# Kernel optimization log

Hardware: AMD Instinct MI355X
Metric: run time of the kernel (lower is better)

The kernel has to match this reference:

```python
import jax, jax.numpy as jnp
import numpy as np

B, S, F = 4096, 128, 256

def setup_inputs() -> dict:
    key = jax.random.key(0)
    k0, k1, k2 = jax.random.split(key, 3)
    token_embeds = jax.random.normal(k0, (B, S, F), dtype=jnp.float32)
    attention_mask = jax.random.randint(k1, (B, S), 0, 2).astype(jnp.bool_)
    kw1, kw2 = jax.random.split(k2)
    scale = 1.0 / np.sqrt(F)
    W1 = jax.random.uniform(kw1, (F, F), minval=-scale, maxval=scale, dtype=jnp.float32)
    W2 = jax.random.uniform(kw2, (F, F), minval=-scale, maxval=scale, dtype=jnp.float32)
    b1 = jnp.zeros((F,), jnp.float32)
    b2 = jnp.zeros((F,), jnp.float32)
    return {"token_embeds": token_embeds, "attention_mask": attention_mask,
            "W1": W1, "b1": b1, "W2": W2, "b2": b2}

def reference(token_embeds, attention_mask, W1, b1, W2, b2):
    # masked sum pooling over tokens: [B,S,F] * [B,S,1] -> sum over S -> [B,F]
    mask = attention_mask.astype(token_embeds.dtype)[:, :, None]
    x = jnp.einsum('bsf,bs->bf', token_embeds, mask[:, :, 0])
    # linear1 + tanh (dropout is identity in eval mode)
    x = jnp.tanh(x @ W1.T + b1)
    x = jnp.tanh(x @ W2.T + b2)
    return x
```

## Files before the change

kernel.cpp:

```cpp
#include <hip/hip_runtime.h>
#include <stdint.h>
#include <math.h>

constexpr int S_LEN = 128;
constexpr int F_DIM = 256;
constexpr int F4    = F_DIM / 4;
constexpr int ROWS  = 16;

__global__ __launch_bounds__(256) void pool_kernel(
    const float* __restrict__ te, const void* __restrict__ mask,
    float* __restrict__ xout)
{
  const int t    = threadIdx.x;
  const int wave = t >> 6;
  const int lane = t & 63;
  const long b   = (long)blockIdx.x * 4 + wave;

  const uint32_t* mw = (const uint32_t*)mask;
  uint32_t v = mw[lane];
  unsigned long long isF  = __ballot(v == 0x3F800000u);
  unsigned long long big  = __ballot(v > 1u);
  const int fmt = isF ? 2 : (big ? 1 : 0);

  const float4* te4  = (const float4*)te;
  const long    tb   = b * S_LEN * F4 + lane;
  const long    mb   = b * S_LEN;

  float4 acc = make_float4(0.f, 0.f, 0.f, 0.f);

  if (fmt == 0) {
    const int* mi = (const int*)mask;
    #pragma unroll 4
    for (int s = 0; s < S_LEN; ++s) {
      float  m  = (float)mi[mb + s];
      float4 tv = te4[tb + (long)s * F4];
      acc.x = fmaf(m, tv.x, acc.x); acc.y = fmaf(m, tv.y, acc.y);
      acc.z = fmaf(m, tv.z, acc.z); acc.w = fmaf(m, tv.w, acc.w);
    }
  } else if (fmt == 1) {
    const uint8_t* mu = (const uint8_t*)mask;
    #pragma unroll 4
    for (int s = 0; s < S_LEN; ++s) {
      float  m  = (float)mu[mb + s];
      float4 tv = te4[tb + (long)s * F4];
      acc.x = fmaf(m, tv.x, acc.x); acc.y = fmaf(m, tv.y, acc.y);
      acc.z = fmaf(m, tv.z, acc.z); acc.w = fmaf(m, tv.w, acc.w);
    }
  } else {
    const float* mf = (const float*)mask;
    #pragma unroll 4
    for (int s = 0; s < S_LEN; ++s) {
      float  m  = mf[mb + s];
      float4 tv = te4[tb + (long)s * F4];
      acc.x = fmaf(m, tv.x, acc.x); acc.y = fmaf(m, tv.y, acc.y);
      acc.z = fmaf(m, tv.z, acc.z); acc.w = fmaf(m, tv.w, acc.w);
    }
  }

  ((float4*)xout)[b * F4 + lane] = acc;
}

__global__ __launch_bounds__(256) void mlp_kernel(
    float* __restrict__ x,
    const float* __restrict__ W1, const float* __restrict__ b1,
    const float* __restrict__ W2, const float* __restrict__ b2)
{
  __shared__ float xs[ROWS][F_DIM];
  __shared__ float wt[64][F_DIM];

  const int t    = threadIdx.x;
  const int wave = t >> 6;
  const int lane = t & 63;
  const long rowBase = (long)blockIdx.x * ROWS;
  float4* xg = (float4*)(x + rowBase * F_DIM);

  #pragma unroll
  for (int k = 0; k < (ROWS * F4) / 256; ++k)
    ((float4*)&xs[0][0])[t + 256 * k] = xg[t + 256 * k];
  __syncthreads();

  const int r0 = wave * (ROWS / 4);
  const int c  = lane * 4;

  for (int layer = 0; layer < 2; ++layer) {
    const float* W    = layer ? W2 : W1;
    const float* bias = layer ? b2 : b1;

    float4 bv = ((const float4*)bias)[lane];
    float4 acc[ROWS / 4];
    #pragma unroll
    for (int r = 0; r < ROWS / 4; ++r) acc[r] = bv;

    for (int fc = 0; fc < F_DIM; fc += 64) {
      __syncthreads();
      const float4* wrow = (const float4*)(W + (long)t * F_DIM + fc);
      #pragma unroll
      for (int k = 0; k < 16; ++k) {
        float4 wv = wrow[k];
        wt[4*k + 0][t] = wv.x; wt[4*k + 1][t] = wv.y;
        wt[4*k + 2][t] = wv.z; wt[4*k + 3][t] = wv.w;
      }
      __syncthreads();

      #pragma unroll 8
      for (int f = 0; f < 64; ++f) {
        float4 wv = *(const float4*)&wt[f][c];
        #pragma unroll
        for (int r = 0; r < ROWS / 4; ++r) {
          float xv = xs[r0 + r][fc + f];
          acc[r].x = fmaf(xv, wv.x, acc[r].x);
          acc[r].y = fmaf(xv, wv.y, acc[r].y);
          acc[r].z = fmaf(xv, wv.z, acc[r].z);
          acc[r].w = fmaf(xv, wv.w, acc[r].w);
        }
      }
    }
    __syncthreads();
    #pragma unroll
    for (int r = 0; r < ROWS / 4; ++r) {
      float4 o;
      o.x = tanhf(acc[r].x); o.y = tanhf(acc[r].y);
      o.z = tanhf(acc[r].z); o.w = tanhf(acc[r].w);
      *(float4*)&xs[r0 + r][c] = o;
    }
    __syncthreads();
  }

  #pragma unroll
  for (int k = 0; k < (ROWS * F4) / 256; ++k)
    xg[t + 256 * k] = ((float4*)&xs[0][0])[t + 256 * k];
}

extern "C" void kernel_launch(void* const* d_in, const int* in_sizes, int n_in,
                              void* d_out, int out_size, void* d_ws, size_t ws_size,
                              hipStream_t stream) {
  const float* te   = (const float*)d_in[0];
  const void*  mask = d_in[1];
  const float* W1   = (const float*)d_in[2];
  const float* b1   = (const float*)d_in[3];
  const float* W2   = (const float*)d_in[4];
  const float* b2   = (const float*)d_in[5];
  float* out = (float*)d_out;

  const int Btot = in_sizes[0] / (S_LEN * F_DIM);

  pool_kernel<<<dim3(Btot / 4), dim3(256), 0, stream>>>(te, mask, out);
  mlp_kernel<<<dim3(Btot / ROWS), dim3(256), 0, stream>>>(out, W1, b1, W2, b2);
}
```

Before: 724.1 us.

## Gather only unmasked tokens in pooling and pre-transpose weights for MLP

```diff
diff --git a/kernel.cpp b/kernel.cpp
--- a/kernel.cpp
+++ b/kernel.cpp
@@ -7,128 +7,134 @@
 constexpr int F4    = F_DIM / 4;
 constexpr int ROWS  = 16;
 
+__device__ __forceinline__ int mbcnt64(unsigned long long m) {
+  return __builtin_amdgcn_mbcnt_hi((unsigned)(m >> 32),
+         __builtin_amdgcn_mbcnt_lo((unsigned)(m & 0xffffffffu), 0));
+}
+__device__ __forceinline__ void add4(float4& a, const float4 b) {
+  a.x += b.x; a.y += b.y; a.z += b.z; a.w += b.w;
+}
+__device__ __forceinline__ void fma4(float4& a, float s, const float4 w) {
+  a.x = fmaf(s, w.x, a.x); a.y = fmaf(s, w.y, a.y);
+  a.z = fmaf(s, w.z, a.z); a.w = fmaf(s, w.w, a.w);
+}
+
+__global__ __launch_bounds__(256) void wt_kernel(
+    const float* __restrict__ W1, const float* __restrict__ W2,
+    float* __restrict__ wsT)
+{
+  int id  = blockIdx.x * 256 + threadIdx.x;
+  int mat = id >> 16;
+  int o   = id & 65535;
+  int f   = o >> 8, j = o & 255;
+  const float* W = mat ? W2 : W1;
+  wsT[(mat << 16) + o] = W[j * 256 + f];
+}
+
 __global__ __launch_bounds__(256) void pool_kernel(
     const float* __restrict__ te, const void* __restrict__ mask,
     float* __restrict__ xout)
 {
-  const int t    = threadIdx.x;
-  const int wave = t >> 6;
-  const int lane = t & 63;
-  const long b   = (long)blockIdx.x * 4 + wave;
+  __shared__ int sl[4][132];
+
+  const int t = threadIdx.x, w = t >> 6, l = t & 63;
+  const long b = (long)blockIdx.x * 4 + w;
 
   const uint32_t* mw = (const uint32_t*)mask;
-  uint32_t v = mw[lane];
-  unsigned long long isF  = __ballot(v == 0x3F800000u);
-  unsigned long long big  = __ballot(v > 1u);
-  const int fmt = isF ? 2 : (big ? 1 : 0);
+  uint32_t v = mw[l];
+  const int fmt = __ballot(v == 0x3F800000u) ? 2 : (__ballot(v > 1u) ? 1 : 0);
 
-  const float4* te4  = (const float4*)te;
-  const long    tb   = b * S_LEN * F4 + lane;
-  const long    mb   = b * S_LEN;
+  bool a0, a1;
+  if (fmt == 0) {
+    const int* m = (const int*)mask + b * S_LEN;
+    a0 = m[l] != 0; a1 = m[64 + l] != 0;
+  } else if (fmt == 1) {
+    const uint8_t* m = (const uint8_t*)mask + b * S_LEN;
+    a0 = m[l] != 0; a1 = m[64 + l] != 0;
+  } else {
+    const float* m = (const float*)mask + b * S_LEN;
+    a0 = m[l] != 0.f; a1 = m[64 + l] != 0.f;
+  }
+  unsigned long long b0 = __ballot(a0), b1 = __ballot(a1);
+  const int c0 = __popcll(b0);
+  const int cnt = c0 + __popcll(b1);
+  if (a0) sl[w][mbcnt64(b0)]      = l;
+  if (a1) sl[w][c0 + mbcnt64(b1)] = 64 + l;
+  __syncthreads();
 
+  const float4* src = (const float4*)te + b * (S_LEN * F4) + l;
   float4 acc = make_float4(0.f, 0.f, 0.f, 0.f);
 
-  if (fmt == 0) {
-    const int* mi = (const int*)mask;
-    #pragma unroll 4
-    for (int s = 0; s < S_LEN; ++s) {
-      float  m  = (float)mi[mb + s];
-      float4 tv = te4[tb + (long)s * F4];
-      acc.x = fmaf(m, tv.x, acc.x); acc.y = fmaf(m, tv.y, acc.y);
-      acc.z = fmaf(m, tv.z, acc.z); acc.w = fmaf(m, tv.w, acc.w);
-    }
-  } else if (fmt == 1) {
-    const uint8_t* mu = (const uint8_t*)mask;
-    #pragma unroll 4
-    for (int s = 0; s < S_LEN; ++s) {
-      float  m  = (float)mu[mb + s];
-      float4 tv = te4[tb + (long)s * F4];
-      acc.x = fmaf(m, tv.x, acc.x); acc.y = fmaf(m, tv.y, acc.y);
-      acc.z = fmaf(m, tv.z, acc.z); acc.w = fmaf(m, tv.w, acc.w);
-    }
-  } else {
-    const float* mf = (const float*)mask;
-    #pragma unroll 4
-    for (int s = 0; s < S_LEN; ++s) {
-      float  m  = mf[mb + s];
-      float4 tv = te4[tb + (long)s * F4];
-      acc.x = fmaf(m, tv.x, acc.x); acc.y = fmaf(m, tv.y, acc.y);
-      acc.z = fmaf(m, tv.z, acc.z); acc.w = fmaf(m, tv.w, acc.w);
-    }
+  int i = 0;
+  for (; i + 8 <= cnt; i += 8) {
+    int s0 = sl[w][i+0], s1 = sl[w][i+1], s2 = sl[w][i+2], s3 = sl[w][i+3];
+    int s4 = sl[w][i+4], s5 = sl[w][i+5], s6 = sl[w][i+6], s7 = sl[w][i+7];
+    float4 t0 = src[s0*F4], t1 = src[s1*F4], t2 = src[s2*F4], t3 = src[s3*F4];
+    float4 t4 = src[s4*F4], t5 = src[s5*F4], t6 = src[s6*F4], t7 = src[s7*F4];
+    add4(t0, t1); add4(t2, t3); add4(t4, t5); add4(t6, t7);
+    add4(t0, t2); add4(t4, t6); add4(t0, t4); add4(acc, t0);
   }
+  for (; i < cnt; ++i) add4(acc, src[sl[w][i] * F4]);
 
-  ((float4*)xout)[b * F4 + lane] = acc;
+  ((float4*)xout)[b * F4 + l] = acc;
 }
 
 __global__ __launch_bounds__(256) void mlp_kernel(
-    float* __restrict__ x,
-    const float* __restrict__ W1, const float* __restrict__ b1,
-    const float* __restrict__ W2, const float* __restrict__ b2)
+    float* __restrict__ x, const float* __restrict__ wsT,
+    const float* __restrict__ b1, const float* __restrict__ b2)
 {
   __shared__ float xs[ROWS][F_DIM];
   __shared__ float wt[64][F_DIM];
 
-  const int t    = threadIdx.x;
-  const int wave = t >> 6;
-  const int lane = t & 63;
+  const int t = threadIdx.x, w = t >> 6, l = t & 63;
   const long rowBase = (long)blockIdx.x * ROWS;
   float4* xg = (float4*)(x + rowBase * F_DIM);
 
   #pragma unroll
   for (int k = 0; k < (ROWS * F4) / 256; ++k)
-    ((float4*)&xs[0][0])[t + 256 * k] = xg[t + 256 * k];
+    ((float4*)xs)[t + 256 * k] = xg[t + 256 * k];
   __syncthreads();
 
-  const int r0 = wave * (ROWS / 4);
-  const int c  = lane * 4;
+  const int r0 = w * 4;
+  const int c  = l * 4;
 
   for (int layer = 0; layer < 2; ++layer) {
-    const float* W    = layer ? W2 : W1;
+    const float* Wt   = wsT + layer * 65536;
     const float* bias = layer ? b2 : b1;
 
-    float4 bv = ((const float4*)bias)[lane];
-    float4 acc[ROWS / 4];
-    #pragma unroll
-    for (int r = 0; r < ROWS / 4; ++r) acc[r] = bv;
+    float4 bv = ((const float4*)bias)[l];
+    float4 acc0 = bv, acc1 = bv, acc2 = bv, acc3 = bv;
 
     for (int fc = 0; fc < F_DIM; fc += 64) {
       __syncthreads();
-      const float4* wrow = (const float4*)(W + (long)t * F_DIM + fc);
+      const float4* src = (const float4*)(Wt + fc * F_DIM);
       #pragma unroll
-      for (int k = 0; k < 16; ++k) {
-        float4 wv = wrow[k];
-        wt[4*k + 0][t] = wv.x; wt[4*k + 1][t] = wv.y;
-        wt[4*k + 2][t] = wv.z; wt[4*k + 3][t] = wv.w;
-      }
+      for (int k = 0; k < 16; ++k)
+        ((float4*)wt)[t + 256 * k] = src[t + 256 * k];
       __syncthreads();
 
       #pragma unroll 8
       for (int f = 0; f < 64; ++f) {
         float4 wv = *(const float4*)&wt[f][c];
-        #pragma unroll
-        for (int r = 0; r < ROWS / 4; ++r) {
-          float xv = xs[r0 + r][fc + f];
-          acc[r].x = fmaf(xv, wv.x, acc[r].x);
-          acc[r].y = fmaf(xv, wv.y, acc[r].y);
-          acc[r].z = fmaf(xv, wv.z, acc[r].z);
-          acc[r].w = fmaf(xv, wv.w, acc[r].w);
-        }
+        float x0 = xs[r0+0][fc+f], x1 = xs[r0+1][fc+f];
+        float x2 = xs[r0+2][fc+f], x3 = xs[r0+3][fc+f];
+        fma4(acc0, x0, wv); fma4(acc1, x1, wv);
+        fma4(acc2, x2, wv); fma4(acc3, x3, wv);
       }
     }
+    float4 o0, o1, o2, o3;
+    o0.x=tanhf(acc0.x); o0.y=tanhf(acc0.y); o0.z=tanhf(acc0.z); o0.w=tanhf(acc0.w);
+    o1.x=tanhf(acc1.x); o1.y=tanhf(acc1.y); o1.z=tanhf(acc1.z); o1.w=tanhf(acc1.w);
+    o2.x=tanhf(acc2.x); o2.y=tanhf(acc2.y); o2.z=tanhf(acc2.z); o2.w=tanhf(acc2.w);
+    o3.x=tanhf(acc3.x); o3.y=tanhf(acc3.y); o3.z=tanhf(acc3.z); o3.w=tanhf(acc3.w);
     __syncthreads();
-    #pragma unroll
-    for (int r = 0; r < ROWS / 4; ++r) {
-      float4 o;
-      o.x = tanhf(acc[r].x); o.y = tanhf(acc[r].y);
-      o.z = tanhf(acc[r].z); o.w = tanhf(acc[r].w);
-      *(float4*)&xs[r0 + r][c] = o;
-    }
-    __syncthreads();
+    *(float4*)&xs[r0+0][c] = o0; *(float4*)&xs[r0+1][c] = o1;
+    *(float4*)&xs[r0+2][c] = o2; *(float4*)&xs[r0+3][c] = o3;
   }
-
+  __syncthreads();
   #pragma unroll
   for (int k = 0; k < (ROWS * F4) / 256; ++k)
-    xg[t + 256 * k] = ((float4*)&xs[0][0])[t + 256 * k];
+    xg[t + 256 * k] = ((float4*)xs)[t + 256 * k];
 }
 
 extern "C" void kernel_launch(void* const* d_in, const int* in_sizes, int n_in,
@@ -140,10 +146,12 @@
   const float* b1   = (const float*)d_in[3];
   const float* W2   = (const float*)d_in[4];
   const float* b2   = (const float*)d_in[5];
-  float* out = (float*)d_out;
+  float* out  = (float*)d_out;
+  float* wsT  = (float*)d_ws;
 
   const int Btot = in_sizes[0] / (S_LEN * F_DIM);
 
-  pool_kernel<<<dim3(Btot / 4), dim3(256), 0, stream>>>(te, mask, out);
-  mlp_kernel<<<dim3(Btot / ROWS), dim3(256), 0, stream>>>(out, W1, b1, W2, b2);
+  wt_kernel  <<<dim3(512),        dim3(256), 0, stream>>>(W1, W2, wsT);
+  pool_kernel<<<dim3(Btot / 4),   dim3(256), 0, stream>>>(te, mask, out);
+  mlp_kernel <<<dim3(Btot / ROWS), dim3(256), 0, stream>>>(out, wsT, b1, b2);
 }
```

New measurement: 671.6 us. 1.08x faster.
